# Kernel tuning notes

Measured on AMD Instinct MI355X. Metric: run time of the kernel, lower is better.

The kernel has to match this reference:

```python
import jax, jax.numpy as jnp
import numpy as np

N = 200_000          # nodes
E = 6_400_000        # directed edges (before self loops)
F_IN, F_OUT = 20, 10
NEG_SLOPE = 0.2      # PyG GATConv default
BN_EPS = 1e-5


def setup_inputs() -> dict:
    key = jax.random.key(0)
    ks = jax.random.split(key, 20)
    s = 0.1
    return {
        "h": jax.random.normal(ks[0], (N, F_IN), jnp.float32),
        "edge_index": jax.random.randint(ks[1], (2, E), 0, N, dtype=jnp.int64),
        "edge_weight": jax.random.uniform(ks[2], (E, 1), dtype=jnp.float32),
        # BatchNorm1d(20) affine params
        "bn_w": jnp.ones((F_IN,), jnp.float32),
        "bn_b": jnp.zeros((F_IN,), jnp.float32),
        # GATConv params (heads=1): lin (no bias), att vectors, edge lin, output bias
        "W": jax.random.normal(ks[3], (F_OUT, F_IN), jnp.float32) * s,
        "att_src": jax.random.normal(ks[4], (F_OUT,), jnp.float32) * s,
        "att_dst": jax.random.normal(ks[5], (F_OUT,), jnp.float32) * s,
        "att_edge": jax.random.normal(ks[6], (F_OUT,), jnp.float32) * s,
        "W_edge": jax.random.normal(ks[7], (F_OUT, 1), jnp.float32) * s,
        "bias": jax.random.normal(ks[8], (F_OUT,), jnp.float32) * s,
        # dense MLP
        "fc1_w": jax.random.normal(ks[9], (F_OUT, F_OUT), jnp.float32) * s,
        "fc1_b": jnp.zeros((F_OUT,), jnp.float32),
        "fc2_w": jax.random.normal(ks[10], (F_OUT, F_OUT), jnp.float32) * s,
        "fc2_b": jnp.zeros((F_OUT,), jnp.float32),
        "fc3_w": jax.random.normal(ks[11], (F_OUT, F_OUT), jnp.float32) * s,
        "fc3_b": jnp.zeros((F_OUT,), jnp.float32),
    }


def reference(h, edge_index, edge_weight, bn_w, bn_b, W, att_src, att_dst,
              att_edge, W_edge, bias, fc1_w, fc1_b, fc2_w, fc2_b, fc3_w, fc3_b):
    # --- BatchNorm1d (training mode: batch stats, biased variance) ---
    mu = h.mean(axis=0)
    var = jnp.var(h, axis=0)
    xn = (h - mu) * jax.lax.rsqrt(var + BN_EPS) * bn_w + bn_b   # [N, 20]

    # --- GATConv (heads=1, edge_dim=1, add_self_loops, fill_value='mean') ---
    xp = xn @ W.T                       # [N, 10] projected node features
    a_s = xp @ att_src                  # [N] per-node source attention term
    a_d = xp @ att_dst                  # [N] per-node dest attention term

    loop = jnp.arange(N, dtype=edge_index.dtype)
    src = jnp.concatenate([edge_index[0], loop])          # [E+N]
    dst = jnp.concatenate([edge_index[1], loop])          # [E+N]
    loop_attr = jnp.broadcast_to(edge_weight.mean(axis=0), (N, 1))
    ea = jnp.concatenate([edge_weight, loop_attr], axis=0)  # [E+N, 1]

    a_e = (ea @ W_edge.T) @ att_edge                       # [E+N]
    logits = jax.nn.leaky_relu(a_s[src] + a_d[dst] + a_e, NEG_SLOPE)

    # segment softmax over destination neighborhoods (every node has a self loop)
    m = jax.ops.segment_max(logits, dst, num_segments=N)
    ex = jnp.exp(logits - m[dst])
    denom = jax.ops.segment_sum(ex, dst, num_segments=N)
    alpha = ex / denom[dst]                                # [E+N]

    msg = xp[src] * alpha[:, None]                         # [E+N, 10]
    out = jax.ops.segment_sum(msg, dst, num_segments=N) + bias  # [N, 10]

    embeddings = jax.nn.relu(out)
    y = jax.nn.relu(out @ fc1_w.T + fc1_b)
    y = jax.nn.relu(y @ fc2_w.T + fc2_b)
    y = y @ fc3_w.T + fc3_b
    return embeddings, y
```

## Files before the change

### kernel.cpp

```cpp
#include <hip/hip_runtime.h>
#include <hip/hip_fp16.h>

#define NN 200000
#define NE 6400000
#define F_IN 20
#define F_OUT 10
#define NEG_SLOPE 0.2f
#define BN_EPS 1e-5f

#define NPB 256
#define NBUCK 782
#define CHUNK 8192
#define NBLK 782
#define SB 512
#define NPT (CHUNK / SB)
#define SZ (NBUCK * NBLK)
#define SCANB 1024
#define G1 ((SZ + SCANB - 1) / SCANB)
#define HSB 240
#define RT 1024
#define MAXB 9216
#define CNPT ((MAXB + RT - 1) / RT)

#define OFF_C      41
#define OFF_LOOPAE 42
#define OFF_SCALE  64
#define OFF_SHIFT  84
#define OFF_PART   128
#define OFF_PEW    (OFF_PART + HSB * 40)
#define OFF_AD     (OFF_PEW + HSB)
#define OFF_XPA    (OFF_AD + NN)
#define OFF_XPB    (OFF_XPA + 4 * NN)
#define OFF_SCN    (OFF_XPB + 2 * NN)
#define OFF_BS     (OFF_SCN + SZ + 1)
#define OFF_SCT    (OFF_BS + 1024)
#define OFF_M      (((OFF_SCT + SZ) + 1) & ~1)
#define OFF_REC    OFF_M

typedef unsigned long long u64;

__global__ void k_hstats(const float* __restrict__ h, float* __restrict__ part) {
    float s[F_IN], q[F_IN];
#pragma unroll
    for (int f = 0; f < F_IN; ++f) { s[f] = 0.f; q[f] = 0.f; }
    for (int i = blockIdx.x * blockDim.x + threadIdx.x; i < NN;
         i += gridDim.x * blockDim.x) {
        const float4* row = (const float4*)(h + (size_t)i * F_IN);
#pragma unroll
        for (int v = 0; v < 5; ++v) {
            float4 x = row[v];
            int f = v * 4;
            s[f+0] += x.x; q[f+0] += x.x * x.x;
            s[f+1] += x.y; q[f+1] += x.y * x.y;
            s[f+2] += x.z; q[f+2] += x.z * x.z;
            s[f+3] += x.w; q[f+3] += x.w * x.w;
        }
    }
#pragma unroll
    for (int f = 0; f < F_IN; ++f)
        for (int o = 32; o > 0; o >>= 1) {
            s[f] += __shfl_down(s[f], o);
            q[f] += __shfl_down(q[f], o);
        }
    __shared__ float red[4][40];
    int t = threadIdx.x, wave = t >> 6, lane = t & 63;
    if (lane == 0) {
#pragma unroll
        for (int f = 0; f < F_IN; ++f) { red[wave][f] = s[f]; red[wave][F_IN + f] = q[f]; }
    }
    __syncthreads();
    if (t < 40) part[blockIdx.x * 40 + t] = red[0][t] + red[1][t] + red[2][t] + red[3][t];
}

__global__ void k_ewsum(const float* __restrict__ ew, float* __restrict__ pew) {
    float s = 0.f;
    const float4* e4 = (const float4*)ew;
    const int n4 = NE / 4;
    for (int i = blockIdx.x * blockDim.x + threadIdx.x; i < n4;
         i += gridDim.x * blockDim.x) {
        float4 x = e4[i];
        s += x.x + x.y + x.z + x.w;
    }
    for (int o = 32; o > 0; o >>= 1) s += __shfl_down(s, o);
    __shared__ float red[4];
    int t = threadIdx.x;
    if ((t & 63) == 0) red[t >> 6] = s;
    __syncthreads();
    if (t == 0) pew[blockIdx.x] = red[0] + red[1] + red[2] + red[3];
}

__global__ void k_params(const float* __restrict__ bn_w, const float* __restrict__ bn_b,
                         const float* __restrict__ W_edge, const float* __restrict__ att_edge,
                         const float* __restrict__ part, const float* __restrict__ pew,
                         float* __restrict__ ws) {
    __shared__ float col[40];
    __shared__ float ews;
    int t = threadIdx.x;
    if (t < 40) {
        float s = 0.f;
#pragma unroll 8
        for (int b = 0; b < HSB; ++b) s += part[b * 40 + t];
        col[t] = s;
    }
    if (t == 40) {
        float s = 0.f;
#pragma unroll 8
        for (int b = 0; b < HSB; ++b) s += pew[b];
        ews = s;
    }
    __syncthreads();
    if (t < F_IN) {
        float mu  = col[t] / (float)NN;
        float var = col[F_IN + t] / (float)NN - mu * mu;
        float sc  = bn_w[t] * rsqrtf(var + BN_EPS);
        ws[OFF_SCALE + t] = sc;
        ws[OFF_SHIFT + t] = bn_b[t] - mu * sc;
    }
    if (t == 63) {
        float c = 0.f;
#pragma unroll
        for (int k = 0; k < F_OUT; ++k) c += W_edge[k] * att_edge[k];
        ws[OFF_C] = c;
        ws[OFF_LOOPAE] = c * (ews / (float)NE);
    }
}

__global__ void k_node(const float* __restrict__ h, const float* __restrict__ W,
                       const float* __restrict__ att_src, const float* __restrict__ att_dst,
                       const float* __restrict__ ws_ro, __half* __restrict__ xpa,
                       float* __restrict__ xpb, float* __restrict__ a_d) {
    __shared__ float sW[F_OUT * F_IN], sAs[F_OUT], sAd[F_OUT], sSc[F_IN], sSh[F_IN];
    int t = threadIdx.x;
    if (t < F_OUT * F_IN) sW[t] = W[t];
    if (t < F_OUT) { sAs[t] = att_src[t]; sAd[t] = att_dst[t]; }
    if (t >= 224 && t < 224 + F_IN) {
        sSc[t - 224] = ws_ro[OFF_SCALE + (t - 224)];
        sSh[t - 224] = ws_ro[OFF_SHIFT + (t - 224)];
    }
    __syncthreads();
    int i = blockIdx.x * blockDim.x + t;
    if (i >= NN) return;
    float xn[F_IN];
    const float4* row = (const float4*)(h + (size_t)i * F_IN);
#pragma unroll
    for (int v = 0; v < 5; ++v) {
        float4 x = row[v];
        int f = v * 4;
        xn[f+0] = x.x * sSc[f+0] + sSh[f+0];
        xn[f+1] = x.y * sSc[f+1] + sSh[f+1];
        xn[f+2] = x.z * sSc[f+2] + sSh[f+2];
        xn[f+3] = x.w * sSc[f+3] + sSh[f+3];
    }
    float acc[F_OUT];
    float as = 0.f, ad = 0.f;
#pragma unroll
    for (int k = 0; k < F_OUT; ++k) {
        float a = 0.f;
#pragma unroll
        for (int f = 0; f < F_IN; ++f) a += sW[k * F_IN + f] * xn[f];
        acc[k] = a;
        as += a * sAs[k];
        ad += a * sAd[k];
    }
    __half2 h01 = __floats2half2_rn(acc[0], acc[1]);
    __half2 h23 = __floats2half2_rn(acc[2], acc[3]);
    __half2 h45 = __floats2half2_rn(acc[4], acc[5]);
    __half2 h67 = __floats2half2_rn(acc[6], acc[7]);
    __half2 h89 = __floats2half2_rn(acc[8], acc[9]);
    uint4 U;
    U.x = *(unsigned*)&h01; U.y = *(unsigned*)&h23;
    U.z = *(unsigned*)&h45; U.w = *(unsigned*)&h67;
    *(uint4*)(xpa + (size_t)i * 8) = U;
    uint2 V;
    V.x = *(unsigned*)&h89;
    V.y = __float_as_uint(as);
    *(uint2*)(xpb + (size_t)i * 2) = V;
    a_d[i] = ad;
}

__global__ void __launch_bounds__(SB) k_bcount(const int* __restrict__ ei, int* __restrict__ M) {
    __shared__ int hist[NBUCK];
    int t = threadIdx.x, blk = blockIdx.x;
    for (int i = t; i < NBUCK; i += SB) hist[i] = 0;
    __syncthreads();
    int base = blk * CHUNK;
    int lim = NE - base; if (lim > CHUNK) lim = CHUNK;
    for (int j = t; j < lim; j += SB) {
        int dst = ei[NE + base + j];
        atomicAdd(&hist[dst >> 8], 1);
    }
    __syncthreads();
    for (int i = t; i < NBUCK; i += SB) M[i * NBLK + blk] = hist[i];
}

__global__ void k_scan1(const int* __restrict__ M, int* __restrict__ SCN,
                        int* __restrict__ BS) {
    __shared__ int tmp[SCANB];
    int t = threadIdx.x, g = blockIdx.x;
    int idx = g * SCANB + t;
    int v = (idx < SZ) ? M[idx] : 0;
    tmp[t] = v;
    __syncthreads();
    for (int off = 1; off < SCANB; off <<= 1) {
        int x = (t >= off) ? tmp[t - off] : 0;
        __syncthreads();
        tmp[t] += x;
        __syncthreads();
    }
    if (idx < SZ) SCN[idx] = tmp[t] - v;
    if (t == SCANB - 1) BS[g] = tmp[t];
}

__global__ void k_scan2(int* __restrict__ BS, int* __restrict__ SCN) {
    __shared__ int tmp[SCANB];
    int t = threadIdx.x;
    int v = (t < G1) ? BS[t] : 0;
    tmp[t] = v;
    __syncthreads();
    for (int off = 1; off < SCANB; off <<= 1) {
        int x = (t >= off) ? tmp[t - off] : 0;
        __syncthreads();
        tmp[t] += x;
        __syncthreads();
    }
    if (t < G1) BS[t] = tmp[t] - v;
    if (t == 0) SCN[SZ] = NE;
}

__global__ void k_scan3(int* __restrict__ SCN, const int* __restrict__ BS,
                        int* __restrict__ SCT) {
    int idx = blockIdx.x * SCANB + threadIdx.x;
    if (idx < SZ) {
        int v = SCN[idx] + BS[blockIdx.x];
        SCN[idx] = v;
        int b   = idx / NBLK;
        int blk = idx - b * NBLK;
        SCT[blk * NBUCK + b] = v;
    }
}

__global__ void __launch_bounds__(SB) k_scatter(
        const int* __restrict__ ei, const float* __restrict__ ew,
        const int* __restrict__ SCT, u64* __restrict__ rec) {
    __shared__ u64 sBuf[CHUNK];
    __shared__ int sScan[1024];
    __shared__ int sCur[NBUCK];
    __shared__ int sBase[NBUCK];
    int t = threadIdx.x, blk = blockIdx.x;
    sScan[t] = 0; sScan[t + SB] = 0;
    for (int i = t; i < NBUCK; i += SB) sBase[i] = SCT[blk * NBUCK + i];
    __syncthreads();
    int base = blk * CHUNK;
    int lim = NE - base; if (lim > CHUNK) lim = CHUNK;
    u64 r[NPT]; int bk[NPT];
#pragma unroll
    for (int k = 0; k < NPT; ++k) {
        int j = t + k * SB;
        bk[k] = -1;
        if (j < lim) {
            int e = base + j;
            int src = __builtin_nontemporal_load(ei + e);
            int dst = ei[NE + e];
            float w  = __builtin_nontemporal_load(ew + e);
            int b = dst >> 8;
            bk[k] = b;
            r[k] = ((u64)__float_as_uint(w) << 32) |
                   (u64)(((unsigned)src << 8) | (unsigned)(dst & (NPB - 1)));
            atomicAdd(&sScan[b], 1);
        }
    }
    __syncthreads();
    for (int d = 1; d < 1024; d <<= 1) {
        int idx = (t + 1) * (d << 1) - 1;
        if (idx < 1024) sScan[idx] += sScan[idx - d];
        __syncthreads();
    }
    if (t == 0) sScan[1023] = 0;
    __syncthreads();
    for (int d = 512; d >= 1; d >>= 1) {
        int idx = (t + 1) * (d << 1) - 1;
        if (idx < 1024) {
            int x = sScan[idx - d];
            sScan[idx - d] = sScan[idx];
            sScan[idx] += x;
        }
        __syncthreads();
    }
    for (int i = t; i < NBUCK; i += SB) sCur[i] = sScan[i];
    __syncthreads();
#pragma unroll
    for (int k = 0; k < NPT; ++k) {
        if (bk[k] >= 0) {
            int p = atomicAdd(&sCur[bk[k]], 1);
            sBuf[p] = r[k];
        }
    }
    __syncthreads();
    int grp = t >> 3, lane = t & 7;
    for (int b = grp; b < NBUCK; b += SB / 8) {
        int st = sScan[b];
        int len = sScan[b + 1] - st;
        int gb = sBase[b];
        for (int k2 = lane; k2 < len; k2 += 8)
            rec[gb + k2] = sBuf[st + k2];
    }
}

__global__ void __launch_bounds__(RT, 8) k_creduce(
        const float* __restrict__ ws_ro, const int* __restrict__ SCN,
        const u64* __restrict__ rec, const __half* __restrict__ xpa,
        const float* __restrict__ xpb, const float* __restrict__ a_d,
        const float* __restrict__ bias,
        const float* __restrict__ fc1w, const float* __restrict__ fc1b,
        const float* __restrict__ fc2w, const float* __restrict__ fc2b,
        const float* __restrict__ fc3w, const float* __restrict__ fc3b,
        float* __restrict__ out) {
    __shared__ u64 sBuf[MAXB];
    __shared__ int sHist[NPB];
    __shared__ int sOff[NPB + 1];
    __shared__ float s1[100], s2[100], s3[100], sb[F_OUT], sb1[F_OUT], sb2[F_OUT], sb3[F_OUT];
    int t = threadIdx.x, b = blockIdx.x;
    if (t < NPB) sHist[t] = 0;
    if (t < 100) { s1[t] = fc1w[t]; s2[t] = fc2w[t]; s3[t] = fc3w[t]; }
    if (t >= 256 && t < 256 + F_OUT) {
        int k = t - 256;
        sb[k] = bias[k]; sb1[k] = fc1b[k]; sb2[k] = fc2b[k]; sb3[k] = fc3b[k];
    }
    __syncthreads();
    int start = SCN[b * NBLK];
    int cnt = SCN[(b + 1) * NBLK] - start;
    if (cnt > MAXB) cnt = MAXB;
    u64 r[CNPT];
#pragma unroll
    for (int k = 0; k < CNPT; ++k) {
        int i = t + k * RT;
        if (i < cnt) {
            r[k] = __builtin_nontemporal_load(rec + start + i);
            atomicAdd(&sHist[(unsigned)r[k] & (NPB - 1u)], 1);
        }
    }
    __syncthreads();
    int v = (t < NPB) ? sHist[t] : 0;
    for (int off = 1; off < NPB; off <<= 1) {
        int x = (t >= off && t < NPB) ? sHist[t - off] : 0;
        __syncthreads();
        if (t < NPB) sHist[t] += x;
        __syncthreads();
    }
    if (t < NPB) { sOff[t + 1] = sHist[t]; sHist[t] -= v; }
    if (t == 0) sOff[0] = 0;
    __syncthreads();
#pragma unroll
    for (int k = 0; k < CNPT; ++k) {
        int i = t + k * RT;
        if (i < cnt) {
            int p = atomicAdd(&sHist[(unsigned)r[k] & (NPB - 1u)], 1);
            if (p < MAXB) sBuf[p] = r[k];
        }
    }
    __syncthreads();
    int node = t & (NPB - 1);
    int quarter = t >> 8;
    int gnode = b * NPB + node;
    float adn = (gnode < NN) ? a_d[gnode] : 0.f;
    float c = ws_ro[OFF_C];
    const uint4* xpa4 = (const uint4*)xpa;
    const uint2* xpb2 = (const uint2*)xpb;
    int myStart = sOff[node];
    int e0 = sOff[node + 1];
    float den = 0.f;
    float num[F_OUT];
#pragma unroll
    for (int k = 0; k < F_OUT; ++k) num[k] = 0.f;
    int j = myStart + quarter;
    for (; j + 12 < e0; j += 16) {
        u64 r1 = sBuf[j];
        u64 r2 = sBuf[j + 4];
        u64 r3 = sBuf[j + 8];
        u64 r4 = sBuf[j + 12];
        unsigned i1 = (unsigned)r1 >> 8, i2 = (unsigned)r2 >> 8;
        unsigned i3 = (unsigned)r3 >> 8, i4 = (unsigned)r4 >> 8;
        uint4 A1 = xpa4[i1]; uint4 A2 = xpa4[i2];
        uint4 A3 = xpa4[i3]; uint4 A4 = xpa4[i4];
        uint2 B1 = xpb2[i1]; uint2 B2 = xpb2[i2];
        uint2 B3 = xpb2[i3]; uint2 B4 = xpb2[i4];
        float l1 = __uint_as_float(B1.y) + adn + c * __uint_as_float((unsigned)(r1 >> 32));
        float l2 = __uint_as_float(B2.y) + adn + c * __uint_as_float((unsigned)(r2 >> 32));
        float l3 = __uint_as_float(B3.y) + adn + c * __uint_as_float((unsigned)(r3 >> 32));
        float l4 = __uint_as_float(B4.y) + adn + c * __uint_as_float((unsigned)(r4 >> 32));
        l1 = l1 > 0.f ? l1 : NEG_SLOPE * l1;
        l2 = l2 > 0.f ? l2 : NEG_SLOPE * l2;
        l3 = l3 > 0.f ? l3 : NEG_SLOPE * l3;
        l4 = l4 > 0.f ? l4 : NEG_SLOPE * l4;
        float e1 = __expf(l1), e2 = __expf(l2), e3 = __expf(l3), e4 = __expf(l4);
        float2 f0 = __half22float2(*(const __half2*)&A1.x);
        float2 f1 = __half22float2(*(const __half2*)&A1.y);
        float2 f2 = __half22float2(*(const __half2*)&A1.z);
        float2 f3 = __half22float2(*(const __half2*)&A1.w);
        float2 f4 = __half22float2(*(const __half2*)&B1.x);
        float2 g0 = __half22float2(*(const __half2*)&A2.x);
        float2 g1 = __half22float2(*(const __half2*)&A2.y);
        float2 g2 = __half22float2(*(const __half2*)&A2.z);
        float2 g3 = __half22float2(*(const __half2*)&A2.w);
        float2 g4 = __half22float2(*(const __half2*)&B2.x);
        float2 h0 = __half22float2(*(const __half2*)&A3.x);
        float2 h1 = __half22float2(*(const __half2*)&A3.y);
        float2 h2 = __half22float2(*(const __half2*)&A3.z);
        float2 h3 = __half22float2(*(const __half2*)&A3.w);
        float2 h4 = __half22float2(*(const __half2*)&B3.x);
        float2 k0 = __half22float2(*(const __half2*)&A4.x);
        float2 k1 = __half22float2(*(const __half2*)&A4.y);
        float2 k2 = __half22float2(*(const __half2*)&A4.z);
        float2 k3 = __half22float2(*(const __half2*)&A4.w);
        float2 k4 = __half22float2(*(const __half2*)&B4.x);
        den += (e1 + e2) + (e3 + e4);
        num[0] += e1 * f0.x + e2 * g0.x + e3 * h0.x + e4 * k0.x;
        num[1] += e1 * f0.y + e2 * g0.y + e3 * h0.y + e4 * k0.y;
        num[2] += e1 * f1.x + e2 * g1.x + e3 * h1.x + e4 * k1.x;
        num[3] += e1 * f1.y + e2 * g1.y + e3 * h1.y + e4 * k1.y;
        num[4] += e1 * f2.x + e2 * g2.x + e3 * h2.x + e4 * k2.x;
        num[5] += e1 * f2.y + e2 * g2.y + e3 * h2.y + e4 * k2.y;
        num[6] += e1 * f3.x + e2 * g3.x + e3 * h3.x + e4 * k3.x;
        num[7] += e1 * f3.y + e2 * g3.y + e3 * h3.y + e4 * k3.y;
        num[8] += e1 * f4.x + e2 * g4.x + e3 * h4.x + e4 * k4.x;
        num[9] += e1 * f4.y + e2 * g4.y + e3 * h4.y + e4 * k4.y;
    }
    for (; j < e0; j += 4) {
        u64 r1 = sBuf[j];
        unsigned i1 = (unsigned)r1 >> 8;
        uint4 A = xpa4[i1];
        uint2 B = xpb2[i1];
        float l1 = __uint_as_float(B.y) + adn + c * __uint_as_float((unsigned)(r1 >> 32));
        l1 = l1 > 0.f ? l1 : NEG_SLOPE * l1;
        float e1 = __expf(l1);
        float2 f0 = __half22float2(*(const __half2*)&A.x);
        float2 f1 = __half22float2(*(const __half2*)&A.y);
        float2 f2 = __half22float2(*(const __half2*)&A.z);
        float2 f3 = __half22float2(*(const __half2*)&A.w);
        float2 f4 = __half22float2(*(const __half2*)&B.x);
        den += e1;
        num[0] += e1 * f0.x; num[1] += e1 * f0.y;
        num[2] += e1 * f1.x; num[3] += e1 * f1.y;
        num[4] += e1 * f2.x; num[5] += e1 * f2.y;
        num[6] += e1 * f3.x; num[7] += e1 * f3.y;
        num[8] += e1 * f4.x; num[9] += e1 * f4.y;
    }
    __syncthreads();
    float* sP = (float*)sBuf;
    if (quarter) {
        float* p = sP + (node * 3 + (quarter - 1)) * 11;
        p[0] = den;
#pragma unroll
        for (int k = 0; k < F_OUT; ++k) p[1 + k] = num[k];
    }
    __syncthreads();
    if (quarter) return;
#pragma unroll
    for (int q = 0; q < 3; ++q) {
        const float* p = sP + (node * 3 + q) * 11;
        den += p[0];
#pragma unroll
        for (int k = 0; k < F_OUT; ++k) num[k] += p[1 + k];
    }

    if (gnode >= NN) return;
    uint4 An = xpa4[gnode];
    uint2 Bn = xpb2[gnode];
    float l = __uint_as_float(Bn.y) + adn + ws_ro[OFF_LOOPAE];
    l = l > 0.f ? l : NEG_SLOPE * l;
    float exs = __expf(l);
    float inv = 1.0f / (den + exs);
    float xn[F_OUT];
    {
        float2 f0 = __half22float2(*(const __half2*)&An.x);
        float2 f1 = __half22float2(*(const __half2*)&An.y);
        float2 f2 = __half22float2(*(const __half2*)&An.z);
        float2 f3 = __half22float2(*(const __half2*)&An.w);
        float2 f4 = __half22float2(*(const __half2*)&Bn.x);
        xn[0]=f0.x; xn[1]=f0.y; xn[2]=f1.x; xn[3]=f1.y; xn[4]=f2.x;
        xn[5]=f2.y; xn[6]=f3.x; xn[7]=f3.y; xn[8]=f4.x; xn[9]=f4.y;
    }
    float o[F_OUT], y1[F_OUT], y2[F_OUT];
#pragma unroll
    for (int k = 0; k < F_OUT; ++k) {
        o[k] = (num[k] + exs * xn[k]) * inv + sb[k];
        out[(size_t)gnode * F_OUT + k] = fmaxf(o[k], 0.f);
    }
#pragma unroll
    for (int k = 0; k < F_OUT; ++k) {
        float a = sb1[k];
#pragma unroll
        for (int jj = 0; jj < F_OUT; ++jj) a += s1[k * F_OUT + jj] * o[jj];
        y1[k] = fmaxf(a, 0.f);
    }
#pragma unroll
    for (int k = 0; k < F_OUT; ++k) {
        float a = sb2[k];
#pragma unroll
        for (int jj = 0; jj < F_OUT; ++jj) a += s2[k * F_OUT + jj] * y1[jj];
        y2[k] = fmaxf(a, 0.f);
    }
#pragma unroll
    for (int k = 0; k < F_OUT; ++k) {
        float a = sb3[k];
#pragma unroll
        for (int jj = 0; jj < F_OUT; ++jj) a += s3[k * F_OUT + jj] * y2[jj];
        out[(size_t)NN * F_OUT + (size_t)gnode * F_OUT + k] = a;
    }
}

extern "C" void kernel_launch(void* const* d_in, const int* in_sizes, int n_in,
                              void* d_out, int out_size, void* d_ws, size_t ws_size,
                              hipStream_t stream) {
    const float* h        = (const float*)d_in[0];
    const int*   ei       = (const int*)  d_in[1];
    const float* ew       = (const float*)d_in[2];
    const float* bn_w     = (const float*)d_in[3];
    const float* bn_b     = (const float*)d_in[4];
    const float* W        = (const float*)d_in[5];
    const float* att_src  = (const float*)d_in[6];
    const float* att_dst  = (const float*)d_in[7];
    const float* att_edge = (const float*)d_in[8];
    const float* W_edge   = (const float*)d_in[9];
    const float* bias     = (const float*)d_in[10];
    const float* fc1w     = (const float*)d_in[11];
    const float* fc1b     = (const float*)d_in[12];
    const float* fc2w     = (const float*)d_in[13];
    const float* fc2b     = (const float*)d_in[14];
    const float* fc3w     = (const float*)d_in[15];
    const float* fc3b     = (const float*)d_in[16];
    float* ws  = (float*)d_ws;
    int*   wsi = (int*)d_ws;
    float* out = (float*)d_out;
    __half* xpa = (__half*)(ws + OFF_XPA);
    float*  xpb = ws + OFF_XPB;

    k_hstats<<<HSB, 256, 0, stream>>>(h, ws + OFF_PART);
    k_ewsum <<<HSB, 256, 0, stream>>>(ew, ws + OFF_PEW);
    k_params<<<1, 64, 0, stream>>>(bn_w, bn_b, W_edge, att_edge,
                                   ws + OFF_PART, ws + OFF_PEW, ws);
    k_node  <<<(NN + 255) / 256, 256, 0, stream>>>(h, W, att_src, att_dst, ws,
                                                   xpa, xpb, ws + OFF_AD);
    k_bcount<<<NBLK, SB, 0, stream>>>(ei, wsi + OFF_M);
    k_scan1 <<<G1, SCANB, 0, stream>>>(wsi + OFF_M, wsi + OFF_SCN, wsi + OFF_BS);
    k_scan2 <<<1, SCANB, 0, stream>>>(wsi + OFF_BS, wsi + OFF_SCN);
    k_scan3 <<<G1, SCANB, 0, stream>>>(wsi + OFF_SCN, wsi + OFF_BS, wsi + OFF_SCT);
    k_scatter<<<NBLK, SB, 0, stream>>>(ei, ew, wsi + OFF_SCT, (u64*)(wsi + OFF_REC));
    k_creduce<<<NBUCK, RT, 0, stream>>>(ws, wsi + OFF_SCN, (const u64*)(wsi + OFF_REC),
                                        xpa, xpb, ws + OFF_AD,
                                        bias, fc1w, fc1b, fc2w, fc2b, fc3w, fc3b, out);
}
```

Baseline: 355.5 us.

## Replace count+scan bucket partition with atomic per-bucket slots in fixed-capacity regions

```diff
diff --git a/kernel.cpp b/kernel.cpp
--- a/kernel.cpp
+++ b/kernel.cpp
@@ -14,9 +14,6 @@
 #define NBLK 782
 #define SB 512
 #define NPT (CHUNK / SB)
-#define SZ (NBUCK * NBLK)
-#define SCANB 1024
-#define G1 ((SZ + SCANB - 1) / SCANB)
 #define HSB 240
 #define RT 1024
 #define MAXB 9216
@@ -31,11 +28,8 @@
 #define OFF_AD     (OFF_PEW + HSB)
 #define OFF_XPA    (OFF_AD + NN)
 #define OFF_XPB    (OFF_XPA + 4 * NN)
-#define OFF_SCN    (OFF_XPB + 2 * NN)
-#define OFF_BS     (OFF_SCN + SZ + 1)
-#define OFF_SCT    (OFF_BS + 1024)
-#define OFF_M      (((OFF_SCT + SZ) + 1) & ~1)
-#define OFF_REC    OFF_M
+#define OFF_CNT    (OFF_XPB + 2 * NN)
+#define OFF_REC    (((OFF_CNT + NBUCK) + 1) & ~1)
 
 typedef unsigned long long u64;
 
@@ -128,9 +122,12 @@
 __global__ void k_node(const float* __restrict__ h, const float* __restrict__ W,
                        const float* __restrict__ att_src, const float* __restrict__ att_dst,
                        const float* __restrict__ ws_ro, __half* __restrict__ xpa,
-                       float* __restrict__ xpb, float* __restrict__ a_d) {
+                       float* __restrict__ xpb, float* __restrict__ a_d,
+                       int* __restrict__ gcnt) {
     __shared__ float sW[F_OUT * F_IN], sAs[F_OUT], sAd[F_OUT], sSc[F_IN], sSh[F_IN];
     int t = threadIdx.x;
+    if (blockIdx.x == 0)
+        for (int i = t; i < NBUCK; i += 256) gcnt[i] = 0;
     if (t < F_OUT * F_IN) sW[t] = W[t];
     if (t < F_OUT) { sAs[t] = att_src[t]; sAd[t] = att_dst[t]; }
     if (t >= 224 && t < 224 + F_IN) {
@@ -178,77 +175,14 @@
     a_d[i] = ad;
 }
 
-__global__ void __launch_bounds__(SB) k_bcount(const int* __restrict__ ei, int* __restrict__ M) {
-    __shared__ int hist[NBUCK];
-    int t = threadIdx.x, blk = blockIdx.x;
-    for (int i = t; i < NBUCK; i += SB) hist[i] = 0;
-    __syncthreads();
-    int base = blk * CHUNK;
-    int lim = NE - base; if (lim > CHUNK) lim = CHUNK;
-    for (int j = t; j < lim; j += SB) {
-        int dst = ei[NE + base + j];
-        atomicAdd(&hist[dst >> 8], 1);
-    }
-    __syncthreads();
-    for (int i = t; i < NBUCK; i += SB) M[i * NBLK + blk] = hist[i];
-}
-
-__global__ void k_scan1(const int* __restrict__ M, int* __restrict__ SCN,
-                        int* __restrict__ BS) {
-    __shared__ int tmp[SCANB];
-    int t = threadIdx.x, g = blockIdx.x;
-    int idx = g * SCANB + t;
-    int v = (idx < SZ) ? M[idx] : 0;
-    tmp[t] = v;
-    __syncthreads();
-    for (int off = 1; off < SCANB; off <<= 1) {
-        int x = (t >= off) ? tmp[t - off] : 0;
-        __syncthreads();
-        tmp[t] += x;
-        __syncthreads();
-    }
-    if (idx < SZ) SCN[idx] = tmp[t] - v;
-    if (t == SCANB - 1) BS[g] = tmp[t];
-}
-
-__global__ void k_scan2(int* __restrict__ BS, int* __restrict__ SCN) {
-    __shared__ int tmp[SCANB];
-    int t = threadIdx.x;
-    int v = (t < G1) ? BS[t] : 0;
-    tmp[t] = v;
-    __syncthreads();
-    for (int off = 1; off < SCANB; off <<= 1) {
-        int x = (t >= off) ? tmp[t - off] : 0;
-        __syncthreads();
-        tmp[t] += x;
-        __syncthreads();
-    }
-    if (t < G1) BS[t] = tmp[t] - v;
-    if (t == 0) SCN[SZ] = NE;
-}
-
-__global__ void k_scan3(int* __restrict__ SCN, const int* __restrict__ BS,
-                        int* __restrict__ SCT) {
-    int idx = blockIdx.x * SCANB + threadIdx.x;
-    if (idx < SZ) {
-        int v = SCN[idx] + BS[blockIdx.x];
-        SCN[idx] = v;
-        int b   = idx / NBLK;
-        int blk = idx - b * NBLK;
-        SCT[blk * NBUCK + b] = v;
-    }
-}
-
 __global__ void __launch_bounds__(SB) k_scatter(
         const int* __restrict__ ei, const float* __restrict__ ew,
-        const int* __restrict__ SCT, u64* __restrict__ rec) {
+        int* __restrict__ gcnt, u64* __restrict__ rec) {
     __shared__ u64 sBuf[CHUNK];
     __shared__ int sScan[1024];
     __shared__ int sCur[NBUCK];
-    __shared__ int sBase[NBUCK];
     int t = threadIdx.x, blk = blockIdx.x;
     sScan[t] = 0; sScan[t + SB] = 0;
-    for (int i = t; i < NBUCK; i += SB) sBase[i] = SCT[blk * NBUCK + i];
     __syncthreads();
     int base = blk * CHUNK;
     int lim = NE - base; if (lim > CHUNK) lim = CHUNK;
@@ -300,14 +234,20 @@
     for (int b = grp; b < NBUCK; b += SB / 8) {
         int st = sScan[b];
         int len = sScan[b + 1] - st;
-        int gb = sBase[b];
-        for (int k2 = lane; k2 < len; k2 += 8)
-            rec[gb + k2] = sBuf[st + k2];
+        if (len == 0) continue;
+        int gb0 = 0;
+        if (lane == 0) gb0 = atomicAdd(&gcnt[b], len);
+        int gb = __shfl(gb0, 0, 8);
+        int avail = MAXB - gb;
+        int cplen = len < avail ? len : (avail > 0 ? avail : 0);
+        u64* dst = rec + (size_t)b * MAXB + gb;
+        for (int k2 = lane; k2 < cplen; k2 += 8)
+            dst[k2] = sBuf[st + k2];
     }
 }
 
 __global__ void __launch_bounds__(RT, 8) k_creduce(
-        const float* __restrict__ ws_ro, const int* __restrict__ SCN,
+        const float* __restrict__ ws_ro, const int* __restrict__ gcnt,
         const u64* __restrict__ rec, const __half* __restrict__ xpa,
         const float* __restrict__ xpb, const float* __restrict__ a_d,
         const float* __restrict__ bias,
@@ -327,8 +267,8 @@
         sb[k] = bias[k]; sb1[k] = fc1b[k]; sb2[k] = fc2b[k]; sb3[k] = fc3b[k];
     }
     __syncthreads();
-    int start = SCN[b * NBLK];
-    int cnt = SCN[(b + 1) * NBLK] - start;
+    int start = b * MAXB;
+    int cnt = gcnt[b];
     if (cnt > MAXB) cnt = MAXB;
     u64 r[CNPT];
 #pragma unroll
@@ -534,19 +474,17 @@
     float* out = (float*)d_out;
     __half* xpa = (__half*)(ws + OFF_XPA);
     float*  xpb = ws + OFF_XPB;
+    int*    gcnt = wsi + OFF_CNT;
+    u64*    rec = (u64*)(wsi + OFF_REC);
 
     k_hstats<<<HSB, 256, 0, stream>>>(h, ws + OFF_PART);
     k_ewsum <<<HSB, 256, 0, stream>>>(ew, ws + OFF_PEW);
     k_params<<<1, 64, 0, stream>>>(bn_w, bn_b, W_edge, att_edge,
                                    ws + OFF_PART, ws + OFF_PEW, ws);
     k_node  <<<(NN + 255) / 256, 256, 0, stream>>>(h, W, att_src, att_dst, ws,
-                                                   xpa, xpb, ws + OFF_AD);
-    k_bcount<<<NBLK, SB, 0, stream>>>(ei, wsi + OFF_M);
-    k_scan1 <<<G1, SCANB, 0, stream>>>(wsi + OFF_M, wsi + OFF_SCN, wsi + OFF_BS);
-    k_scan2 <<<1, SCANB, 0, stream>>>(wsi + OFF_BS, wsi + OFF_SCN);
-    k_scan3 <<<G1, SCANB, 0, stream>>>(wsi + OFF_SCN, wsi + OFF_BS, wsi + OFF_SCT);
-    k_scatter<<<NBLK, SB, 0, stream>>>(ei, ew, wsi + OFF_SCT, (u64*)(wsi + OFF_REC));
-    k_creduce<<<NBUCK, RT, 0, stream>>>(ws, wsi + OFF_SCN, (const u64*)(wsi + OFF_REC),
+                                                   xpa, xpb, ws + OFF_AD, gcnt);
+    k_scatter<<<NBLK, SB, 0, stream>>>(ei, ew, gcnt, rec);
+    k_creduce<<<NBUCK, RT, 0, stream>>>(ws, gcnt, rec,
                                         xpa, xpb, ws + OFF_AD,
                                         bias, fc1w, fc1b, fc2w, fc2b, fc3w, fc3b, out);
 }
```

Measured after the change: 375.2 us. 1.06x slower.

## Fuse stats, edge-weight sum and bucket count; drop scan fixup kernel

Applied to the files above, without the earlier changes.

```diff
diff --git a/kernel.cpp b/kernel.cpp
--- a/kernel.cpp
+++ b/kernel.cpp
@@ -17,7 +17,7 @@
 #define SZ (NBUCK * NBLK)
 #define SCANB 1024
 #define G1 ((SZ + SCANB - 1) / SCANB)
-#define HSB 240
+#define PREB 120
 #define RT 1024
 #define MAXB 9216
 #define CNPT ((MAXB + RT - 1) / RT)
@@ -27,66 +27,90 @@
 #define OFF_SCALE  64
 #define OFF_SHIFT  84
 #define OFF_PART   128
-#define OFF_PEW    (OFF_PART + HSB * 40)
-#define OFF_AD     (OFF_PEW + HSB)
+#define OFF_PEW    (OFF_PART + PREB * 40)
+#define OFF_AD     (OFF_PEW + PREB)
 #define OFF_XPA    (OFF_AD + NN)
 #define OFF_XPB    (OFF_XPA + 4 * NN)
 #define OFF_SCN    (OFF_XPB + 2 * NN)
 #define OFF_BS     (OFF_SCN + SZ + 1)
-#define OFF_SCT    (OFF_BS + 1024)
-#define OFF_M      (((OFF_SCT + SZ) + 1) & ~1)
+#define OFF_M      (((OFF_BS + 1024) + 1) & ~1)
 #define OFF_REC    OFF_M
 
 typedef unsigned long long u64;
 
-__global__ void k_hstats(const float* __restrict__ h, float* __restrict__ part) {
-    float s[F_IN], q[F_IN];
-#pragma unroll
-    for (int f = 0; f < F_IN; ++f) { s[f] = 0.f; q[f] = 0.f; }
-    for (int i = blockIdx.x * blockDim.x + threadIdx.x; i < NN;
-         i += gridDim.x * blockDim.x) {
-        const float4* row = (const float4*)(h + (size_t)i * F_IN);
-#pragma unroll
-        for (int v = 0; v < 5; ++v) {
-            float4 x = row[v];
-            int f = v * 4;
-            s[f+0] += x.x; q[f+0] += x.x * x.x;
-            s[f+1] += x.y; q[f+1] += x.y * x.y;
-            s[f+2] += x.z; q[f+2] += x.z * x.z;
-            s[f+3] += x.w; q[f+3] += x.w * x.w;
-        }
-    }
-#pragma unroll
-    for (int f = 0; f < F_IN; ++f)
-        for (int o = 32; o > 0; o >>= 1) {
-            s[f] += __shfl_down(s[f], o);
-            q[f] += __shfl_down(q[f], o);
-        }
-    __shared__ float red[4][40];
-    int t = threadIdx.x, wave = t >> 6, lane = t & 63;
-    if (lane == 0) {
-#pragma unroll
-        for (int f = 0; f < F_IN; ++f) { red[wave][f] = s[f]; red[wave][F_IN + f] = q[f]; }
-    }
-    __syncthreads();
-    if (t < 40) part[blockIdx.x * 40 + t] = red[0][t] + red[1][t] + red[2][t] + red[3][t];
-}
-
-__global__ void k_ewsum(const float* __restrict__ ew, float* __restrict__ pew) {
-    float s = 0.f;
-    const float4* e4 = (const float4*)ew;
-    const int n4 = NE / 4;
-    for (int i = blockIdx.x * blockDim.x + threadIdx.x; i < n4;
-         i += gridDim.x * blockDim.x) {
-        float4 x = e4[i];
-        s += x.x + x.y + x.z + x.w;
-    }
-    for (int o = 32; o > 0; o >>= 1) s += __shfl_down(s, o);
-    __shared__ float red[4];
+__global__ void __launch_bounds__(SB) k_pre(
+        const float* __restrict__ h, const float* __restrict__ ew,
+        const int* __restrict__ ei, float* __restrict__ part,
+        float* __restrict__ pew, int* __restrict__ M) {
     int t = threadIdx.x;
-    if ((t & 63) == 0) red[t >> 6] = s;
-    __syncthreads();
-    if (t == 0) pew[blockIdx.x] = red[0] + red[1] + red[2] + red[3];
+    if (blockIdx.x < PREB) {
+        float s[F_IN], q[F_IN];
+#pragma unroll
+        for (int f = 0; f < F_IN; ++f) { s[f] = 0.f; q[f] = 0.f; }
+        for (int i = blockIdx.x * SB + t; i < NN; i += PREB * SB) {
+            const float4* row = (const float4*)(h + (size_t)i * F_IN);
+#pragma unroll
+            for (int v = 0; v < 5; ++v) {
+                float4 x = row[v];
+                int f = v * 4;
+                s[f+0] += x.x; q[f+0] += x.x * x.x;
+                s[f+1] += x.y; q[f+1] += x.y * x.y;
+                s[f+2] += x.z; q[f+2] += x.z * x.z;
+                s[f+3] += x.w; q[f+3] += x.w * x.w;
+            }
+        }
+#pragma unroll
+        for (int f = 0; f < F_IN; ++f)
+            for (int o = 32; o > 0; o >>= 1) {
+                s[f] += __shfl_down(s[f], o);
+                q[f] += __shfl_down(q[f], o);
+            }
+        __shared__ float red[8][40];
+        int wave = t >> 6, lane = t & 63;
+        if (lane == 0) {
+#pragma unroll
+            for (int f = 0; f < F_IN; ++f) { red[wave][f] = s[f]; red[wave][F_IN + f] = q[f]; }
+        }
+        __syncthreads();
+        if (t < 40) {
+            float a = 0.f;
+#pragma unroll
+            for (int w8 = 0; w8 < 8; ++w8) a += red[w8][t];
+            part[blockIdx.x * 40 + t] = a;
+        }
+    } else if (blockIdx.x < 2 * PREB) {
+        int g = blockIdx.x - PREB;
+        float s = 0.f;
+        const float4* e4 = (const float4*)ew;
+        const int n4 = NE / 4;
+        for (int i = g * SB + t; i < n4; i += PREB * SB) {
+            float4 x = e4[i];
+            s += x.x + x.y + x.z + x.w;
+        }
+        for (int o = 32; o > 0; o >>= 1) s += __shfl_down(s, o);
+        __shared__ float red2[8];
+        if ((t & 63) == 0) red2[t >> 6] = s;
+        __syncthreads();
+        if (t == 0) {
+            float a = 0.f;
+#pragma unroll
+            for (int w8 = 0; w8 < 8; ++w8) a += red2[w8];
+            pew[g] = a;
+        }
+    } else {
+        __shared__ int hist[NBUCK];
+        int blk = blockIdx.x - 2 * PREB;
+        for (int i = t; i < NBUCK; i += SB) hist[i] = 0;
+        __syncthreads();
+        int base = blk * CHUNK;
+        int lim = NE - base; if (lim > CHUNK) lim = CHUNK;
+        for (int j = t; j < lim; j += SB) {
+            int dst = ei[NE + base + j];
+            atomicAdd(&hist[dst >> 8], 1);
+        }
+        __syncthreads();
+        for (int i = t; i < NBUCK; i += SB) M[i * NBLK + blk] = hist[i];
+    }
 }
 
 __global__ void k_params(const float* __restrict__ bn_w, const float* __restrict__ bn_b,
@@ -99,13 +123,13 @@
     if (t < 40) {
         float s = 0.f;
 #pragma unroll 8
-        for (int b = 0; b < HSB; ++b) s += part[b * 40 + t];
+        for (int b = 0; b < PREB; ++b) s += part[b * 40 + t];
         col[t] = s;
     }
     if (t == 40) {
         float s = 0.f;
 #pragma unroll 8
-        for (int b = 0; b < HSB; ++b) s += pew[b];
+        for (int b = 0; b < PREB; ++b) s += pew[b];
         ews = s;
     }
     __syncthreads();
@@ -178,21 +202,6 @@
     a_d[i] = ad;
 }
 
-__global__ void __launch_bounds__(SB) k_bcount(const int* __restrict__ ei, int* __restrict__ M) {
-    __shared__ int hist[NBUCK];
-    int t = threadIdx.x, blk = blockIdx.x;
-    for (int i = t; i < NBUCK; i += SB) hist[i] = 0;
-    __syncthreads();
-    int base = blk * CHUNK;
-    int lim = NE - base; if (lim > CHUNK) lim = CHUNK;
-    for (int j = t; j < lim; j += SB) {
-        int dst = ei[NE + base + j];
-        atomicAdd(&hist[dst >> 8], 1);
-    }
-    __syncthreads();
-    for (int i = t; i < NBUCK; i += SB) M[i * NBLK + blk] = hist[i];
-}
-
 __global__ void k_scan1(const int* __restrict__ M, int* __restrict__ SCN,
                         int* __restrict__ BS) {
     __shared__ int tmp[SCANB];
@@ -211,7 +220,7 @@
     if (t == SCANB - 1) BS[g] = tmp[t];
 }
 
-__global__ void k_scan2(int* __restrict__ BS, int* __restrict__ SCN) {
+__global__ void k_scan2(int* __restrict__ BS) {
     __shared__ int tmp[SCANB];
     int t = threadIdx.x;
     int v = (t < G1) ? BS[t] : 0;
@@ -224,31 +233,22 @@
         __syncthreads();
     }
     if (t < G1) BS[t] = tmp[t] - v;
-    if (t == 0) SCN[SZ] = NE;
-}
-
-__global__ void k_scan3(int* __restrict__ SCN, const int* __restrict__ BS,
-                        int* __restrict__ SCT) {
-    int idx = blockIdx.x * SCANB + threadIdx.x;
-    if (idx < SZ) {
-        int v = SCN[idx] + BS[blockIdx.x];
-        SCN[idx] = v;
-        int b   = idx / NBLK;
-        int blk = idx - b * NBLK;
-        SCT[blk * NBUCK + b] = v;
-    }
 }
 
 __global__ void __launch_bounds__(SB) k_scatter(
         const int* __restrict__ ei, const float* __restrict__ ew,
-        const int* __restrict__ SCT, u64* __restrict__ rec) {
+        const int* __restrict__ SCN, const int* __restrict__ BS,
+        u64* __restrict__ rec) {
     __shared__ u64 sBuf[CHUNK];
     __shared__ int sScan[1024];
     __shared__ int sCur[NBUCK];
     __shared__ int sBase[NBUCK];
     int t = threadIdx.x, blk = blockIdx.x;
     sScan[t] = 0; sScan[t + SB] = 0;
-    for (int i = t; i < NBUCK; i += SB) sBase[i] = SCT[blk * NBUCK + i];
+    for (int i = t; i < NBUCK; i += SB) {
+        int idx = i * NBLK + blk;
+        sBase[i] = SCN[idx] + BS[idx >> 10];
+    }
     __syncthreads();
     int base = blk * CHUNK;
     int lim = NE - base; if (lim > CHUNK) lim = CHUNK;
@@ -308,6 +308,7 @@
 
 __global__ void __launch_bounds__(RT, 8) k_creduce(
         const float* __restrict__ ws_ro, const int* __restrict__ SCN,
+        const int* __restrict__ BS,
         const u64* __restrict__ rec, const __half* __restrict__ xpa,
         const float* __restrict__ xpb, const float* __restrict__ a_d,
         const float* __restrict__ bias,
@@ -327,8 +328,12 @@
         sb[k] = bias[k]; sb1[k] = fc1b[k]; sb2[k] = fc2b[k]; sb3[k] = fc3b[k];
     }
     __syncthreads();
-    int start = SCN[b * NBLK];
-    int cnt = SCN[(b + 1) * NBLK] - start;
+    int i0 = b * NBLK;
+    int start = SCN[i0] + BS[i0 >> 10];
+    int end;
+    if (b == NBUCK - 1) end = NE;
+    else { int i1 = (b + 1) * NBLK; end = SCN[i1] + BS[i1 >> 10]; }
+    int cnt = end - start;
     if (cnt > MAXB) cnt = MAXB;
     u64 r[CNPT];
 #pragma unroll
@@ -535,18 +540,18 @@
     __half* xpa = (__half*)(ws + OFF_XPA);
     float*  xpb = ws + OFF_XPB;
 
-    k_hstats<<<HSB, 256, 0, stream>>>(h, ws + OFF_PART);
-    k_ewsum <<<HSB, 256, 0, stream>>>(ew, ws + OFF_PEW);
+    k_pre   <<<2 * PREB + NBLK, SB, 0, stream>>>(h, ew, ei, ws + OFF_PART,
+                                                 ws + OFF_PEW, wsi + OFF_M);
     k_params<<<1, 64, 0, stream>>>(bn_w, bn_b, W_edge, att_edge,
                                    ws + OFF_PART, ws + OFF_PEW, ws);
     k_node  <<<(NN + 255) / 256, 256, 0, stream>>>(h, W, att_src, att_dst, ws,
                                                    xpa, xpb, ws + OFF_AD);
-    k_bcount<<<NBLK, SB, 0, stream>>>(ei, wsi + OFF_M);
     k_scan1 <<<G1, SCANB, 0, stream>>>(wsi + OFF_M, wsi + OFF_SCN, wsi + OFF_BS);
-    k_scan2 <<<1, SCANB, 0, stream>>>(wsi + OFF_BS, wsi + OFF_SCN);
-    k_scan3 <<<G1, SCANB, 0, stream>>>(wsi + OFF_SCN, wsi + OFF_BS, wsi + OFF_SCT);
-    k_scatter<<<NBLK, SB, 0, stream>>>(ei, ew, wsi + OFF_SCT, (u64*)(wsi + OFF_REC));
-    k_creduce<<<NBUCK, RT, 0, stream>>>(ws, wsi + OFF_SCN, (const u64*)(wsi + OFF_REC),
+    k_scan2 <<<1, SCANB, 0, stream>>>(wsi + OFF_BS);
+    k_scatter<<<NBLK, SB, 0, stream>>>(ei, ew, wsi + OFF_SCN, wsi + OFF_BS,
+                                       (u64*)(wsi + OFF_REC));
+    k_creduce<<<NBUCK, RT, 0, stream>>>(ws, wsi + OFF_SCN, wsi + OFF_BS,
+                                        (const u64*)(wsi + OFF_REC),
                                         xpa, xpb, ws + OFF_AD,
                                         bias, fc1w, fc1b, fc2w, fc2b, fc3w, fc3b, out);
 }
```

Result: faster. 337.4 us (-5.1%).
